# Optimization experiments

Measured on AMD Instinct MI355X. Metric: run time of the kernel, lower is better.

Reference implementation:

```python
import jax, jax.numpy as jnp
import numpy as np

B, T, H, N, V, E = 4, 128, 1024, 300, 50265, 4800


def setup_inputs() -> dict:
    key = jax.random.key(0)
    ks = jax.random.split(key, 20)
    s = 0.02
    inp = {
        "hidden_states": jax.random.normal(ks[0], (B, T, H), jnp.float32),
        "qt": jax.random.normal(ks[1], (B, T, H), jnp.float32),
        "token_embedding": jax.random.normal(ks[2], (B, T, H), jnp.float32),
        "edges": jax.random.randint(ks[3], (B, 2, E), 0, N),
        "nodeidx2bartidx": jax.random.randint(ks[4], (N,), 0, V),
        # Linear params stored as [in, out] (y = x @ W + b), same math as torch Linear.
        "Wg": jax.random.normal(ks[5], (2 * H, V), jnp.float32) * s,
        "bg": jnp.zeros((V,), jnp.float32),
        "Wh": jax.random.normal(ks[6], (H, H), jnp.float32) * s,
        "Ws": jax.random.normal(ks[7], (H, H), jnp.float32) * s,
        "Wx": jax.random.normal(ks[8], (H, H), jnp.float32) * s,
        "bx": jnp.zeros((H,), jnp.float32),
        "Wps": jax.random.normal(ks[9], (H, 1), jnp.float32) * s,
        "bps": jnp.zeros((1,), jnp.float32),
        "Wc": jax.random.normal(ks[10], (2 * H, N), jnp.float32) * s,
        "bc": jnp.zeros((N,), jnp.float32),
        "Wgg": jax.random.normal(ks[11], (2 * H, 1), jnp.float32) * s,
        "bgg": jnp.zeros((1,), jnp.float32),
        "Wmg": jax.random.normal(ks[12], (2 * H, 1), jnp.float32) * s,
        "bmg": jnp.zeros((1,), jnp.float32),
    }
    return inp


def reference(hidden_states, qt, token_embedding, edges, nodeidx2bartidx,
              Wg, bg, Wh, Ws, Wx, bx, Wps, bps, Wc, bc, Wgg, bgg, Wmg, bmg):
    b, t, h = hidden_states.shape
    n = Wc.shape[1]
    dt = hidden_states.dtype

    hq = jnp.concatenate([hidden_states, qt], axis=-1)          # [B,T,2H]
    gen_pro = hq @ Wg + bg                                       # [B,T,V]
    gen_feat = hidden_states @ Wh + qt @ Ws + (token_embedding @ Wx + bx)
    pro_switch = jax.nn.sigmoid(gen_feat @ Wps + bps)            # [B,T,1]
    qe = jnp.concatenate([qt, token_embedding], axis=-1)
    copy_pro = qe @ Wc + bc                                      # [B,T,N]
    gsem_gate = jax.nn.sigmoid(hq @ Wgg + bgg)                   # [B,T,1]
    memory_gate = jax.nn.sigmoid(hq @ Wmg + bmg)                 # [B,T,1]

    # dense per-example adjacency from COO edges (duplicates accumulate, as in sparse->dense)
    bidx = jnp.arange(b)[:, None]
    Graph = jnp.zeros((b, n, n), dt).at[bidx, edges[:, 0, :], edges[:, 1, :]].add(jnp.asarray(1.0, dt))

    # gated memory recurrence over time + graph propagation
    def step(m_prev, xs):
        cp_t, mg_t = xs                                          # [B,N], [B,1]
        m = cp_t * mg_t + m_prev * (1.0 - mg_t)
        g = jnp.einsum('bij,bj->bi', Graph, m)
        return m, g

    cp_tm = jnp.swapaxes(copy_pro, 0, 1)                         # [T,B,N]
    mg_tm = jnp.swapaxes(memory_gate, 0, 1)                      # [T,B,1]
    _, gsem_tm = jax.lax.scan(step, jnp.zeros((b, n), dt), (cp_tm, mg_tm))
    gsem = jnp.swapaxes(gsem_tm, 0, 1)                           # [B,T,N]

    pro_gsem = copy_pro * gsem_gate + gsem * (1.0 - gsem_gate)
    coverage = jax.nn.softmax(pro_gsem * pro_switch, axis=-1).sum(axis=1)  # [B,N]

    # scatter-add node distribution into vocab space
    gsem_pro = jnp.zeros_like(gen_pro).at[:, :, nodeidx2bartidx].add(pro_gsem)
    total_pro = gen_pro * (1.0 - pro_switch) + gsem_pro * pro_switch
    return total_pro, coverage, jnp.squeeze(pro_switch, axis=-1)
```

## Files before the change

kernel.cpp:

```cpp
#include <hip/hip_runtime.h>
#include <hip/hip_bf16.h>
#include <stdint.h>

#define B_ 4
#define T_ 128
#define H_ 1024
#define N_ 300
#define V_ 50265
#define E_ 4800
#define R_ (B_*T_)
#define GK 2048

#define U_OFF     0
#define PS_OFF    3080
#define GG_OFF    3592
#define MG_OFF    4104
#define Z_OFF     4616
#define M_OFF     (Z_OFF + R_*N_)
#define CP_OFF    (M_OFF + R_*N_)
#define GRAPH_OFF (CP_OFF + R_*N_)
#define COV_OFF   (GRAPH_OFF + B_*N_*N_)
#define FLAG_OFF  (COV_OFF + B_*N_)

#define OUT_COV ((size_t)R_*V_)
#define OUT_PS  (OUT_COV + (size_t)B_*N_)

typedef unsigned short ushort_t;
typedef __bf16 bf16x8 __attribute__((ext_vector_type(8)));
typedef float  f32x4  __attribute__((ext_vector_type(4)));
typedef unsigned short ushort8v __attribute__((ext_vector_type(8)));
typedef unsigned short ushort4v __attribute__((ext_vector_type(4)));
typedef float f32x4v __attribute__((ext_vector_type(4)));

__device__ __forceinline__ ushort_t f2bf(float f) {
    unsigned u = __float_as_uint(f);
    unsigned r = (u + 0x7fffu + ((u >> 16) & 1u)) >> 16;
    return (ushort_t)r;
}
template<bool BF> __device__ __forceinline__ float ldv(const void* p, size_t i) {
    if constexpr (BF) {
        unsigned u = ((unsigned)((const ushort_t*)p)[i]) << 16;
        return __uint_as_float(u);
    } else {
        return ((const float*)p)[i];
    }
}
template<bool BF> __device__ __forceinline__ void stv(void* p, size_t i, float v) {
    if constexpr (BF) ((ushort_t*)p)[i] = f2bf(v);
    else              ((float*)p)[i] = v;
}
__device__ __forceinline__ float sigm(float x) { return 1.0f / (1.0f + expf(-x)); }

__global__ void k_probe(const ushort_t* __restrict__ x, int* __restrict__ flag)
{
    if (threadIdx.x == 0 && blockIdx.x == 0) {
        int cnt = 0;
        for (int i = 0; i < 256; ++i) {
            const int e = (x[i] >> 7) & 0xff;
            cnt += (e >= 100 && e <= 140) ? 1 : 0;
        }
        *flag = (cnt > 200) ? 1 : 0;
    }
}

template<bool BF>
__global__ __launch_bounds__(256)
void k_u(const int* __restrict__ flag,
         const void* __restrict__ Wh, const void* __restrict__ Wsm,
         const void* __restrict__ Wx, const void* __restrict__ bx,
         const void* __restrict__ Wps, const void* __restrict__ bps,
         float* __restrict__ u)
{
    if (*flag != (BF ? 1 : 0)) return;
    const int t = threadIdx.x, w = t >> 6, l = t & 63;
    const int row = blockIdx.x * 4 + w;
    if (row > 3072) return;
    float s = 0.f;
    if (row < 3072) {
        const void* W = (row < 1024) ? Wh : (row < 2048) ? Wsm : Wx;
        const size_t k = (size_t)(row & 1023);
        for (int h = l; h < H_; h += 64)
            s += ldv<BF>(W, k*H_ + h) * ldv<BF>(Wps, h);
    } else {
        for (int h = l; h < H_; h += 64)
            s += ldv<BF>(bx, h) * ldv<BF>(Wps, h);
    }
    for (int o = 32; o; o >>= 1) s += __shfl_down(s, o);
    if (l == 0) {
        if (row < 3072) u[row] = s;
        else            u[3072] = s + ldv<BF>(bps, 0);
    }
}

template<bool BF>
__global__ __launch_bounds__(256)
void k_rows(const int* __restrict__ flag,
            const void* __restrict__ hs, const void* __restrict__ qt,
            const void* __restrict__ te, const float* __restrict__ u,
            const void* __restrict__ Wgg, const void* __restrict__ bgg,
            const void* __restrict__ Wmg, const void* __restrict__ bmg,
            float* __restrict__ ps, float* __restrict__ gg, float* __restrict__ mg,
            void* __restrict__ out_ps)
{
    if (*flag != (BF ? 1 : 0)) return;
    const int r = blockIdx.x, t = threadIdx.x;
    const float* uh = u; const float* us = u + 1024; const float* ux = u + 2048;
    float s1 = 0.f, s2 = 0.f, s3 = 0.f;
    for (int k = t; k < H_; k += 256) {
        const float a = ldv<BF>(hs, (size_t)r*H_ + k);
        const float b = ldv<BF>(qt, (size_t)r*H_ + k);
        const float c = ldv<BF>(te, (size_t)r*H_ + k);
        s1 += a*uh[k] + b*us[k] + c*ux[k];
        s2 += a*ldv<BF>(Wgg, k) + b*ldv<BF>(Wgg, H_ + k);
        s3 += a*ldv<BF>(Wmg, k) + b*ldv<BF>(Wmg, H_ + k);
    }
    for (int o = 32; o; o >>= 1) {
        s1 += __shfl_down(s1, o); s2 += __shfl_down(s2, o); s3 += __shfl_down(s3, o);
    }
    __shared__ float red[3][4];
    const int w = t >> 6, l = t & 63;
    if (l == 0) { red[0][w] = s1; red[1][w] = s2; red[2][w] = s3; }
    __syncthreads();
    if (t == 0) {
        const float S1 = red[0][0]+red[0][1]+red[0][2]+red[0][3] + u[3072];
        const float S2 = red[1][0]+red[1][1]+red[1][2]+red[1][3] + ldv<BF>(bgg, 0);
        const float S3 = red[2][0]+red[2][1]+red[2][2]+red[2][3] + ldv<BF>(bmg, 0);
        const float p = sigm(S1);
        ps[r] = p; gg[r] = sigm(S2); mg[r] = sigm(S3);
        stv<BF>(out_ps, r, p);
    }
}

template<int GN_, bool BIG, bool BF>
__global__ __launch_bounds__(256)
void k_gemm(const int* __restrict__ flag,
            const void* __restrict__ A1, const void* __restrict__ A2,
            const void* __restrict__ Bm, const void* __restrict__ bias,
            const float* __restrict__ ps, float* __restrict__ outf,
            void* __restrict__ outh)
{
    if (*flag != (BF ? 1 : 0)) return;
    constexpr int BM = 128, BN = 128, BK = 32, BKp = 40;
    __shared__ ushort_t As[BM*BK];
    __shared__ ushort_t Bs[BN*BKp];
    const int t = threadIdx.x;
    const int w = t >> 6, l = t & 63;
    const int lr = l & 15, lq = l >> 4;
    const int nb = BIG ? blockIdx.y : blockIdx.x;
    const int mb = BIG ? blockIdx.x : blockIdx.y;
    const int bn0 = nb * BN;
    const int bm0 = mb * BM;
    const int wm = (w >> 1) * 64, wn = (w & 1) * 64;

    const int steps = BIG ? (GK/BK) : (GK/BK/4);
    const int kbeg  = BIG ? 0 : blockIdx.z * steps * BK;

    const int hB = t >> 7;
    const int nB = t & 127;
    const int gnB = bn0 + nB;
    const size_t gnClamp = (size_t)((gnB < GN_) ? gnB : (GN_-1));
    const bool gnOk = (gnB < GN_);

    f32x4 acc[4][4] = {};
    const ushort_t* a_rd = As + (wm + lr)*BK  + lq*8;
    const ushort_t* b_rd = Bs + (wn + lr)*BKp + lq*8;

    ushort8v aBufH[2]; f32x4v aBufF[4]; float bv[16];

    auto load_step = [&](int s) {
        const int k0 = kbeg + s*BK;
        const void* Asrc = (k0 < H_) ? A1 : A2;
        const int kk = k0 & (H_ - 1);
        if constexpr (BF) {
            #pragma unroll
            for (int p = 0; p < 2; ++p) {
                const int slot = p*256 + t, m = slot >> 2, sub = slot & 3;
                aBufH[p] = *(const ushort8v*)((const ushort_t*)Asrc +
                             (size_t)(bm0 + m)*H_ + kk + sub*8);
            }
        } else {
            #pragma unroll
            for (int p = 0; p < 4; ++p) {
                const int slot = p*256 + t, m = slot >> 3, sub = slot & 7;
                aBufF[p] = *(const f32x4v*)((const float*)Asrc +
                             (size_t)(bm0 + m)*H_ + kk + sub*4);
            }
        }
        #pragma unroll
        for (int p = 0; p < 16; ++p) {
            const int k = hB*16 + p;
            const float v = ldv<BF>(Bm, (size_t)(k0 + k)*GN_ + gnClamp);
            bv[p] = gnOk ? v : 0.f;
        }
    };

    auto store_step = [&]() {
        if constexpr (BF) {
            #pragma unroll
            for (int p = 0; p < 2; ++p) {
                const int slot = p*256 + t, m = slot >> 2, sub = slot & 3;
                *(ushort8v*)(As + m*BK + sub*8) = aBufH[p];
            }
        } else {
            #pragma unroll
            for (int p = 0; p < 4; ++p) {
                const int slot = p*256 + t, m = slot >> 3, sub = slot & 7;
                ushort4v h4;
                h4[0] = f2bf(aBufF[p][0]); h4[1] = f2bf(aBufF[p][1]);
                h4[2] = f2bf(aBufF[p][2]); h4[3] = f2bf(aBufF[p][3]);
                *(ushort4v*)(As + m*BK + sub*4) = h4;
            }
        }
        ushort8v b0, b1;
        #pragma unroll
        for (int p = 0; p < 8; ++p)  b0[p] = f2bf(bv[p]);
        #pragma unroll
        for (int p = 0; p < 8; ++p)  b1[p] = f2bf(bv[8+p]);
        *(ushort8v*)(Bs + nB*BKp + hB*16)     = b0;
        *(ushort8v*)(Bs + nB*BKp + hB*16 + 8) = b1;
    };

    load_step(0);
    for (int s = 0; s < steps; ++s) {
        __syncthreads();
        store_step();
        __syncthreads();
        if (s + 1 < steps) load_step(s + 1);

        bf16x8 af[4], bfr[4];
        #pragma unroll
        for (int i = 0; i < 4; ++i) af[i]  = *(const bf16x8*)(a_rd + i*16*BK);
        #pragma unroll
        for (int j = 0; j < 4; ++j) bfr[j] = *(const bf16x8*)(b_rd + j*16*BKp);
        #pragma unroll
        for (int i = 0; i < 4; ++i)
            #pragma unroll
            for (int j = 0; j < 4; ++j)
                acc[i][j] = __builtin_amdgcn_mfma_f32_16x16x32_bf16(af[i], bfr[j], acc[i][j], 0, 0, 0);
    }

    if constexpr (BIG) {
        float omp[16];
        #pragma unroll
        for (int i = 0; i < 4; ++i)
            #pragma unroll
            for (int r2 = 0; r2 < 4; ++r2)
                omp[i*4 + r2] = 1.0f - ps[bm0 + wm + i*16 + lq*4 + r2];
        #pragma unroll
        for (int j = 0; j < 4; ++j) {
            const int gcol = bn0 + wn + j*16 + lr;
            if (gcol < GN_) {
                const float bvv = ldv<BF>(bias, gcol);
                #pragma unroll
                for (int i = 0; i < 4; ++i)
                    #pragma unroll
                    for (int r2 = 0; r2 < 4; ++r2) {
                        const int row = bm0 + wm + i*16 + lq*4 + r2;
                        stv<BF>(outh, (size_t)row*GN_ + gcol,
                                (acc[i][j][r2] + bvv) * omp[i*4 + r2]);
                    }
            }
        }
    } else {
        #pragma unroll
        for (int j = 0; j < 4; ++j) {
            const int gcol = bn0 + wn + j*16 + lr;
            if (gcol < GN_) {
                const float bvv = (blockIdx.z == 0) ? ldv<BF>(bias, gcol) : 0.0f;
                #pragma unroll
                for (int i = 0; i < 4; ++i)
                    #pragma unroll
                    for (int r2 = 0; r2 < 4; ++r2) {
                        const int row = bm0 + wm + i*16 + lq*4 + r2;
                        atomicAdd(outf + (size_t)row*GN_ + gcol, acc[i][j][r2] + bvv);
                    }
            }
        }
    }
}

__global__ void k_graph(const int* __restrict__ edges, float* __restrict__ Graph)
{
    const int gid = blockIdx.x * 256 + threadIdx.x;
    if (gid >= B_*E_) return;
    const int b = gid / E_, e = gid - b*E_;
    const int* eb = edges + (size_t)b * 2 * E_;
    const int i = eb[e], j = eb[E_ + e];
    atomicAdd(Graph + (size_t)b*N_*N_ + (size_t)j*N_ + i, 1.0f);
}

__global__ void k_scan(const float* __restrict__ cp, const float* __restrict__ mg,
                       float* __restrict__ M)
{
    const int gid = blockIdx.x * 256 + threadIdx.x;
    if (gid >= B_*N_) return;
    const int b = gid / N_, n = gid - b*N_;
    float m = 0.f;
    for (int tt = 0; tt < T_; ++tt) {
        const int r = b*T_ + tt;
        const float g = mg[r];
        m = cp[(size_t)r*N_ + n]*g + m*(1.f - g);
        M[(size_t)r*N_ + n] = m;
    }
}

__global__ __launch_bounds__(320)
void k_gsem(const float* __restrict__ Graph, const float* __restrict__ M,
            const float* __restrict__ cp, const float* __restrict__ gg,
            const float* __restrict__ ps, float* __restrict__ z,
            float* __restrict__ cov)
{
    const int r = blockIdx.x;
    const int b = r >> 7;
    const int t = threadIdx.x, w = t >> 6, l = t & 63;
    __shared__ float ml[N_];
    __shared__ float red[5];
    if (t < N_) ml[t] = M[(size_t)r*N_ + t];
    __syncthreads();
    float g = 0.f;
    if (t < N_) {
        const float* GT = Graph + (size_t)b*N_*N_ + t;
        #pragma unroll 4
        for (int j = 0; j < N_; ++j) g += GT[j*N_] * ml[j];
    }
    float zv = 0.f;
    if (t < N_) {
        const float ggv = gg[r];
        const float pg = cp[(size_t)r*N_ + t]*ggv + g*(1.f - ggv);
        zv = pg * ps[r];
        z[(size_t)r*N_ + t] = zv;
    }
    float mv = (t < N_) ? zv : -3.0e38f;
    for (int o = 32; o; o >>= 1) mv = fmaxf(mv, __shfl_down(mv, o));
    if (l == 0) red[w] = mv;
    __syncthreads();
    const float bmx = fmaxf(fmaxf(fmaxf(red[0], red[1]), fmaxf(red[2], red[3])), red[4]);
    __syncthreads();
    const float e = (t < N_) ? expf(zv - bmx) : 0.f;
    float sv = e;
    for (int o = 32; o; o >>= 1) sv += __shfl_down(sv, o);
    if (l == 0) red[w] = sv;
    __syncthreads();
    const float tot = red[0] + red[1] + red[2] + red[3] + red[4];
    if (t < N_) atomicAdd(cov + b*N_ + t, e / tot);
}

template<bool BF>
__global__ void k_cov(const int* __restrict__ flag,
                      const float* __restrict__ cov, void* __restrict__ out)
{
    if (*flag != (BF ? 1 : 0)) return;
    const int gid = blockIdx.x * 256 + threadIdx.x;
    if (gid < B_*N_) stv<BF>(out, gid, cov[gid]);
}

template<bool BF>
__global__ __launch_bounds__(256)
void k_fixup(const int* __restrict__ flag, const int* __restrict__ nidx,
             const float* __restrict__ z, void* __restrict__ out)
{
    if (*flag != (BF ? 1 : 0)) return;
    __shared__ int li[N_];
    const int t = threadIdx.x;
    for (int i = t; i < N_; i += 256) li[i] = nidx[i];
    __syncthreads();
    const int gid = blockIdx.x * 256 + t;
    if (gid >= R_*N_) return;
    const int r = gid / N_, n = gid - r*N_;
    const int v = li[n];
    for (int j = 0; j < n; ++j) if (li[j] == v) return;
    float s = z[(size_t)r*N_ + n];
    for (int j = n + 1; j < N_; ++j) if (li[j] == v) s += z[(size_t)r*N_ + j];
    const size_t o = (size_t)r*V_ + v;
    stv<BF>(out, o, ldv<BF>(out, o) + s);
}

extern "C" void kernel_launch(void* const* d_in, const int* in_sizes, int n_in,
                              void* d_out, int out_size, void* d_ws, size_t ws_size,
                              hipStream_t stream)
{
    (void)in_sizes; (void)n_in; (void)out_size; (void)ws_size;
    const void* hs  = d_in[0];
    const void* qt  = d_in[1];
    const void* te  = d_in[2];
    const int*  edg = (const int*)d_in[3];
    const int*  nid = (const int*)d_in[4];
    const void* Wg  = d_in[5];
    const void* bg  = d_in[6];
    const void* Wh  = d_in[7];
    const void* Wsm = d_in[8];
    const void* Wx  = d_in[9];
    const void* bx  = d_in[10];
    const void* Wps = d_in[11];
    const void* bps = d_in[12];
    const void* Wc  = d_in[13];
    const void* bc  = d_in[14];
    const void* Wgg = d_in[15];
    const void* bgg = d_in[16];
    const void* Wmg = d_in[17];
    const void* bmg = d_in[18];
    float* ws = (float*)d_ws;
    int* flag = (int*)(ws + FLAG_OFF);

    k_probe<<<1, 64, 0, stream>>>((const ushort_t*)hs, flag);
    hipMemsetAsync(ws + CP_OFF, 0,
                   (size_t)(R_*N_ + B_*N_*N_ + B_*N_) * sizeof(float), stream);

    k_u<true ><<<769, 256, 0, stream>>>(flag, Wh, Wsm, Wx, bx, Wps, bps, ws + U_OFF);
    k_u<false><<<769, 256, 0, stream>>>(flag, Wh, Wsm, Wx, bx, Wps, bps, ws + U_OFF);
    k_rows<true ><<<R_, 256, 0, stream>>>(flag, hs, qt, te, ws + U_OFF, Wgg, bgg, Wmg, bmg,
                                          ws + PS_OFF, ws + GG_OFF, ws + MG_OFF,
                                          (ushort_t*)d_out + OUT_PS);
    k_rows<false><<<R_, 256, 0, stream>>>(flag, hs, qt, te, ws + U_OFF, Wgg, bgg, Wmg, bmg,
                                          ws + PS_OFF, ws + GG_OFF, ws + MG_OFF,
                                          (float*)d_out + OUT_PS);
    {
        dim3 g((N_ + 127) / 128, 4, 4);
        k_gemm<N_, false, true ><<<g, 256, 0, stream>>>(flag, qt, te, Wc, bc, nullptr,
                                                        ws + CP_OFF, nullptr);
        k_gemm<N_, false, false><<<g, 256, 0, stream>>>(flag, qt, te, Wc, bc, nullptr,
                                                        ws + CP_OFF, nullptr);
    }
    k_graph<<<(B_*E_ + 255)/256, 256, 0, stream>>>(edg, ws + GRAPH_OFF);
    k_scan<<<(B_*N_ + 255)/256, 256, 0, stream>>>(ws + CP_OFF, ws + MG_OFF, ws + M_OFF);
    k_gsem<<<R_, 320, 0, stream>>>(ws + GRAPH_OFF, ws + M_OFF, ws + CP_OFF,
                                   ws + GG_OFF, ws + PS_OFF, ws + Z_OFF, ws + COV_OFF);
    k_cov<true ><<<(B_*N_ + 255)/256, 256, 0, stream>>>(flag, ws + COV_OFF,
                                                        (ushort_t*)d_out + OUT_COV);
    k_cov<false><<<(B_*N_ + 255)/256, 256, 0, stream>>>(flag, ws + COV_OFF,
                                                        (float*)d_out + OUT_COV);
    {
        dim3 g(4, (V_ + 127) / 128, 1);
        k_gemm<V_, true, true ><<<g, 256, 0, stream>>>(flag, hs, qt, Wg, bg, ws + PS_OFF,
                                                       nullptr, d_out);
        k_gemm<V_, true, false><<<g, 256, 0, stream>>>(flag, hs, qt, Wg, bg, ws + PS_OFF,
                                                       nullptr, d_out);
    }
    k_fixup<true ><<<(R_*N_ + 255)/256, 256, 0, stream>>>(flag, nid, ws + Z_OFF, d_out);
    k_fixup<false><<<(R_*N_ + 255)/256, 256, 0, stream>>>(flag, nid, ws + Z_OFF, d_out);
}
```

Before: 1.026 ms.

## Restructure vocab GEMM: full-M tiles, pre-converted bf16 activations, async LDS loads

```diff
diff --git a/kernel.cpp b/kernel.cpp
--- a/kernel.cpp
+++ b/kernel.cpp
@@ -21,6 +21,7 @@
 #define GRAPH_OFF (CP_OFF + R_*N_)
 #define COV_OFF   (GRAPH_OFF + B_*N_*N_)
 #define FLAG_OFF  (COV_OFF + B_*N_)
+#define ABF_OFF   ((FLAG_OFF + 4) & ~3)
 
 #define OUT_COV ((size_t)R_*V_)
 #define OUT_PS  (OUT_COV + (size_t)B_*N_)
@@ -51,6 +52,12 @@
 }
 __device__ __forceinline__ float sigm(float x) { return 1.0f / (1.0f + expf(-x)); }
 
+__device__ __forceinline__ void gload_lds16(const ushort_t* g, ushort_t* l) {
+    __builtin_amdgcn_global_load_lds(
+        (const __attribute__((address_space(1))) unsigned int*)g,
+        (__attribute__((address_space(3))) unsigned int*)l, 16, 0, 0);
+}
+
 __global__ void k_probe(const ushort_t* __restrict__ x, int* __restrict__ flag)
 {
     if (threadIdx.x == 0 && blockIdx.x == 0) {
@@ -61,6 +68,23 @@
         }
         *flag = (cnt > 200) ? 1 : 0;
     }
+}
+
+template<bool BF>
+__global__ __launch_bounds__(256)
+void k_prep(const int* __restrict__ flag, const void* __restrict__ hs,
+            const void* __restrict__ qt, ushort_t* __restrict__ Abf)
+{
+    if (*flag != (BF ? 1 : 0)) return;
+    const int g = blockIdx.x * 256 + threadIdx.x;
+    const int r  = g >> 8;
+    const int kc = (g & 255) * 8;
+    const void* src = (kc < H_) ? hs : qt;
+    const int k = kc & (H_ - 1);
+    ushort8v o;
+    #pragma unroll
+    for (int p = 0; p < 8; ++p) o[p] = f2bf(ldv<BF>(src, (size_t)r*H_ + k + p));
+    *(ushort8v*)(Abf + (size_t)r*GK + kc) = o;
 }
 
 template<bool BF>
@@ -131,13 +155,114 @@
     }
 }
 
-template<int GN_, bool BIG, bool BF>
+template<bool BF>
+__global__ __launch_bounds__(256)
+void k_gbig(const int* __restrict__ flag,
+            const ushort_t* __restrict__ Abf, const void* __restrict__ Bm,
+            const void* __restrict__ bias, const float* __restrict__ ps,
+            void* __restrict__ outh)
+{
+    if (*flag != (BF ? 1 : 0)) return;
+    constexpr int BN = 64, BK = 32, BKp = 40, STEPS = GK / BK;
+    __shared__ ushort_t As[2][512 * BK];
+    __shared__ ushort_t Bs[2][BN * BKp];
+    const int t = threadIdx.x, w = t >> 6, l = t & 63;
+    const int lr = l & 15, lq = l >> 4;
+    const int bn0 = blockIdx.x * BN;
+    const int wm = w * 128;
+
+    const int nB = t & 63, kg = t >> 6;
+    const int gnB = bn0 + nB;
+    const size_t gnClamp = (size_t)((gnB < V_) ? gnB : (V_ - 1));
+    const bool gnOk = (gnB < V_);
+
+    const int aRow = l >> 2;
+    const int aCsrc = (l & 3) ^ ((l >> 3) & 3);
+    const ushort_t* AgBase = Abf + (size_t)wm * GK;
+
+    float bv[8];
+    f32x4 acc[8][4] = {};
+
+    auto loadB = [&](int s) {
+        const int k0 = s * BK + kg * 8;
+        #pragma unroll
+        for (int p = 0; p < 8; ++p) {
+            const float v = ldv<BF>(Bm, (size_t)(k0 + p) * V_ + gnClamp);
+            bv[p] = gnOk ? v : 0.f;
+        }
+    };
+    auto storeB = [&](int buf) {
+        ushort8v b0;
+        #pragma unroll
+        for (int p = 0; p < 8; ++p) b0[p] = f2bf(bv[p]);
+        *(ushort8v*)(&Bs[buf][nB * BKp + kg * 8]) = b0;
+    };
+    auto stageA = [&](int s, int buf) {
+        const int k0 = s * BK;
+        #pragma unroll
+        for (int i = 0; i < 8; ++i) {
+            const int m = i * 16 + aRow;
+            const ushort_t* g = AgBase + (size_t)m * GK + k0 + aCsrc * 8;
+            ushort_t* lp = &As[buf][(wm + i * 16) * BK];
+            gload_lds16(g, lp);
+        }
+    };
+    auto compute = [&](int buf) {
+        const int aswz = (lq ^ ((lr >> 1) & 3)) * 8;
+        const ushort_t* a_rd = &As[buf][(wm + lr) * BK + aswz];
+        const ushort_t* b_rd = &Bs[buf][lr * BKp + lq * 8];
+        bf16x8 bfr[4];
+        #pragma unroll
+        for (int j = 0; j < 4; ++j) bfr[j] = *(const bf16x8*)(b_rd + j * 16 * BKp);
+        #pragma unroll
+        for (int i = 0; i < 8; ++i) {
+            const bf16x8 af = *(const bf16x8*)(a_rd + i * 16 * BK);
+            #pragma unroll
+            for (int j = 0; j < 4; ++j)
+                acc[i][j] = __builtin_amdgcn_mfma_f32_16x16x32_bf16(af, bfr[j], acc[i][j], 0, 0, 0);
+        }
+    };
+
+    loadB(0);
+    stageA(0, 0);
+    storeB(0);
+    __syncthreads();
+    int cur = 0;
+    for (int s = 0; s < STEPS; ++s) {
+        const bool more = (s + 1 < STEPS);
+        if (more) { loadB(s + 1); stageA(s + 1, cur ^ 1); }
+        compute(cur);
+        if (more) {
+            storeB(cur ^ 1);
+            __syncthreads();
+            cur ^= 1;
+        }
+    }
+
+    #pragma unroll
+    for (int j = 0; j < 4; ++j) {
+        const int gcol = bn0 + j * 16 + lr;
+        if (gcol < V_) {
+            const float bvv = ldv<BF>(bias, gcol);
+            #pragma unroll
+            for (int i = 0; i < 8; ++i) {
+                #pragma unroll
+                for (int r2 = 0; r2 < 4; ++r2) {
+                    const int row = wm + i * 16 + lq * 4 + r2;
+                    stv<BF>(outh, (size_t)row * V_ + gcol,
+                            (acc[i][j][r2] + bvv) * (1.0f - ps[row]));
+                }
+            }
+        }
+    }
+}
+
+template<int GN_, bool BF>
 __global__ __launch_bounds__(256)
 void k_gemm(const int* __restrict__ flag,
             const void* __restrict__ A1, const void* __restrict__ A2,
             const void* __restrict__ Bm, const void* __restrict__ bias,
-            const float* __restrict__ ps, float* __restrict__ outf,
-            void* __restrict__ outh)
+            float* __restrict__ outf)
 {
     if (*flag != (BF ? 1 : 0)) return;
     constexpr int BM = 128, BN = 128, BK = 32, BKp = 40;
@@ -146,14 +271,12 @@
     const int t = threadIdx.x;
     const int w = t >> 6, l = t & 63;
     const int lr = l & 15, lq = l >> 4;
-    const int nb = BIG ? blockIdx.y : blockIdx.x;
-    const int mb = BIG ? blockIdx.x : blockIdx.y;
-    const int bn0 = nb * BN;
-    const int bm0 = mb * BM;
+    const int bn0 = blockIdx.x * BN;
+    const int bm0 = blockIdx.y * BM;
     const int wm = (w >> 1) * 64, wn = (w & 1) * 64;
 
-    const int steps = BIG ? (GK/BK) : (GK/BK/4);
-    const int kbeg  = BIG ? 0 : blockIdx.z * steps * BK;
+    const int steps = GK/BK/4;
+    const int kbeg  = blockIdx.z * steps * BK;
 
     const int hB = t >> 7;
     const int nB = t & 127;
@@ -239,42 +362,18 @@
                 acc[i][j] = __builtin_amdgcn_mfma_f32_16x16x32_bf16(af[i], bfr[j], acc[i][j], 0, 0, 0);
     }
 
-    if constexpr (BIG) {
-        float omp[16];
-        #pragma unroll
-        for (int i = 0; i < 4; ++i)
-            #pragma unroll
-            for (int r2 = 0; r2 < 4; ++r2)
-                omp[i*4 + r2] = 1.0f - ps[bm0 + wm + i*16 + lq*4 + r2];
-        #pragma unroll
-        for (int j = 0; j < 4; ++j) {
-            const int gcol = bn0 + wn + j*16 + lr;
-            if (gcol < GN_) {
-                const float bvv = ldv<BF>(bias, gcol);
+    #pragma unroll
+    for (int j = 0; j < 4; ++j) {
+        const int gcol = bn0 + wn + j*16 + lr;
+        if (gcol < GN_) {
+            const float bvv = (blockIdx.z == 0) ? ldv<BF>(bias, gcol) : 0.0f;
+            #pragma unroll
+            for (int i = 0; i < 4; ++i)
                 #pragma unroll
-                for (int i = 0; i < 4; ++i)
-                    #pragma unroll
-                    for (int r2 = 0; r2 < 4; ++r2) {
-                        const int row = bm0 + wm + i*16 + lq*4 + r2;
-                        stv<BF>(outh, (size_t)row*GN_ + gcol,
-                                (acc[i][j][r2] + bvv) * omp[i*4 + r2]);
-                    }
-            }
-        }
-    } else {
-        #pragma unroll
-        for (int j = 0; j < 4; ++j) {
-            const int gcol = bn0 + wn + j*16 + lr;
-            if (gcol < GN_) {
-                const float bvv = (blockIdx.z == 0) ? ldv<BF>(bias, gcol) : 0.0f;
-                #pragma unroll
-                for (int i = 0; i < 4; ++i)
-                    #pragma unroll
-                    for (int r2 = 0; r2 < 4; ++r2) {
-                        const int row = bm0 + wm + i*16 + lq*4 + r2;
-                        atomicAdd(outf + (size_t)row*GN_ + gcol, acc[i][j][r2] + bvv);
-                    }
-            }
+                for (int r2 = 0; r2 < 4; ++r2) {
+                    const int row = bm0 + wm + i*16 + lq*4 + r2;
+                    atomicAdd(outf + (size_t)row*GN_ + gcol, acc[i][j][r2] + bvv);
+                }
         }
     }
 }
@@ -401,11 +500,14 @@
     const void* bmg = d_in[18];
     float* ws = (float*)d_ws;
     int* flag = (int*)(ws + FLAG_OFF);
+    ushort_t* Abf = (ushort_t*)(ws + ABF_OFF);
 
     k_probe<<<1, 64, 0, stream>>>((const ushort_t*)hs, flag);
     hipMemsetAsync(ws + CP_OFF, 0,
                    (size_t)(R_*N_ + B_*N_*N_ + B_*N_) * sizeof(float), stream);
 
+    k_prep<true ><<<512, 256, 0, stream>>>(flag, hs, qt, Abf);
+    k_prep<false><<<512, 256, 0, stream>>>(flag, hs, qt, Abf);
     k_u<true ><<<769, 256, 0, stream>>>(flag, Wh, Wsm, Wx, bx, Wps, bps, ws + U_OFF);
     k_u<false><<<769, 256, 0, stream>>>(flag, Wh, Wsm, Wx, bx, Wps, bps, ws + U_OFF);
     k_rows<true ><<<R_, 256, 0, stream>>>(flag, hs, qt, te, ws + U_OFF, Wgg, bgg, Wmg, bmg,
@@ -416,10 +518,8 @@
                                           (float*)d_out + OUT_PS);
     {
         dim3 g((N_ + 127) / 128, 4, 4);
-        k_gemm<N_, false, true ><<<g, 256, 0, stream>>>(flag, qt, te, Wc, bc, nullptr,
-                                                        ws + CP_OFF, nullptr);
-        k_gemm<N_, false, false><<<g, 256, 0, stream>>>(flag, qt, te, Wc, bc, nullptr,
-                                                        ws + CP_OFF, nullptr);
+        k_gemm<N_, true ><<<g, 256, 0, stream>>>(flag, qt, te, Wc, bc, ws + CP_OFF);
+        k_gemm<N_, false><<<g, 256, 0, stream>>>(flag, qt, te, Wc, bc, ws + CP_OFF);
     }
     k_graph<<<(B_*E_ + 255)/256, 256, 0, stream>>>(edg, ws + GRAPH_OFF);
     k_scan<<<(B_*N_ + 255)/256, 256, 0, stream>>>(ws + CP_OFF, ws + MG_OFF, ws + M_OFF);
@@ -430,11 +530,10 @@
     k_cov<false><<<(B_*N_ + 255)/256, 256, 0, stream>>>(flag, ws + COV_OFF,
                                                         (float*)d_out + OUT_COV);
     {
-        dim3 g(4, (V_ + 127) / 128, 1);
-        k_gemm<V_, true, true ><<<g, 256, 0, stream>>>(flag, hs, qt, Wg, bg, ws + PS_OFF,
-                                                       nullptr, d_out);
-        k_gemm<V_, true, false><<<g, 256, 0, stream>>>(flag, hs, qt, Wg, bg, ws + PS_OFF,
-                                                       nullptr, d_out);
+        k_gbig<true ><<<(V_ + 63)/64, 256, 0, stream>>>(flag, Abf, Wg, bg,
+                                                        ws + PS_OFF, d_out);
+        k_gbig<false><<<(V_ + 63)/64, 256, 0, stream>>>(flag, Abf, Wg, bg,
+                                                        ws + PS_OFF, d_out);
     }
     k_fixup<true ><<<(R_*N_ + 255)/256, 256, 0, stream>>>(flag, nid, ws + Z_OFF, d_out);
     k_fixup<false><<<(R_*N_ + 255)/256, 256, 0, stream>>>(flag, nid, ws + Z_OFF, d_out);
```

Measured after the change: 1.180 ms. 15.0% more time.
